# Optimization experiments

Hardware: AMD Instinct MI355X
Metric: run time of the kernel (lower is better)

## Reference

```python
import jax, jax.numpy as jnp
import numpy as np

NEG_SLOPE = 0.2  # PyG GATConv default LeakyReLU negative slope


def gat_conv(x, src, dst, W, att_src, att_dst, bias, heads, out_ch, concat):
    """PyG-style GATConv (eval mode, self-loops already appended to src/dst)."""
    n = x.shape[0]
    xh = (x @ W).reshape(n, heads, out_ch)          # [N, H, C]
    a_src = jnp.sum(xh * att_src, axis=-1)          # [N, H]
    a_dst = jnp.sum(xh * att_dst, axis=-1)          # [N, H]
    e = jax.nn.leaky_relu(a_src[src] + a_dst[dst], NEG_SLOPE)  # [E, H]
    # segment softmax over edges grouped by destination node
    m = jax.ops.segment_max(e, dst, num_segments=n)
    m = jnp.where(jnp.isfinite(m), m, 0.0)
    ex = jnp.exp(e - m[dst])
    denom = jax.ops.segment_sum(ex, dst, num_segments=n)
    alpha = ex / (denom[dst] + 1e-16)               # [E, H]
    msg = xh[src] * alpha[..., None]                # [E, H, C]
    out = jax.ops.segment_sum(msg, dst, num_segments=n)  # [N, H, C]
    out = out.reshape(n, heads * out_ch) if concat else out.mean(axis=1)
    return out + bias


def setup_inputs() -> dict:
    key = jax.random.key(0)
    ks = jax.random.split(key, 10)
    N, E, IN, OUT = 50000, 600000, 128, 64
    H1, C1 = 2, 2 * OUT   # conv1: heads=2, out=2*out_channels, concat -> 4*OUT
    H2, C2 = 1, OUT       # conv2: heads=1, concat=False
    s = 0.05
    return {
        "x": jax.random.normal(ks[0], (N, IN), dtype=jnp.float32),
        "edge_index": jax.random.randint(ks[1], (2, E), 0, N, dtype=jnp.int64),
        "W1": jax.random.normal(ks[2], (IN, H1 * C1), dtype=jnp.float32) * s,
        "att_src1": jax.random.normal(ks[3], (H1, C1), dtype=jnp.float32) * s,
        "att_dst1": jax.random.normal(ks[4], (H1, C1), dtype=jnp.float32) * s,
        "b1": jnp.zeros((H1 * C1,), dtype=jnp.float32),
        "W2": jax.random.normal(ks[5], (H1 * C1, H2 * C2), dtype=jnp.float32) * s,
        "att_src2": jax.random.normal(ks[6], (H2, C2), dtype=jnp.float32) * s,
        "att_dst2": jax.random.normal(ks[7], (H2, C2), dtype=jnp.float32) * s,
        "b2": jnp.zeros((C2,), dtype=jnp.float32),
    }


def reference(x, edge_index, W1, att_src1, att_dst1, b1, W2, att_src2, att_dst2, b2):
    n = x.shape[0]
    loop = jnp.arange(n, dtype=edge_index.dtype)
    src = jnp.concatenate([edge_index[0], loop])  # add_self_loops=True
    dst = jnp.concatenate([edge_index[1], loop])
    z = gat_conv(x, src, dst, W1, att_src1, att_dst1, b1, heads=2, out_ch=128, concat=True)
    z = jax.nn.relu(z)
    z = gat_conv(z, src, dst, W2, att_src2, att_dst2, b2, heads=1, out_ch=64, concat=False)
    # decode: dot product over original edge_index (no self loops)
    val = jnp.sum(z[edge_index[0]] * z[edge_index[1]], axis=-1)
    return val.reshape(-1)
```

## Files before the change

kernel.cpp:

```cpp
#include <hip/hip_runtime.h>
#include <math.h>

#define IN_F 128
#define F1 256
#define H1 2
#define F2 64
#define NEG 0.2f

typedef _Float16 f16x8 __attribute__((ext_vector_type(8)));
typedef _Float16 f16x4 __attribute__((ext_vector_type(4)));
typedef float f32x4 __attribute__((ext_vector_type(4)));

__global__ __launch_bounds__(256) void gemm1_mfma(
    const _Float16* __restrict__ Gh, const _Float16* __restrict__ Gl,
    const _Float16* __restrict__ Wth, const _Float16* __restrict__ Wtl,
    const float* __restrict__ b1,
    _Float16* __restrict__ zh, _Float16* __restrict__ zl, int N)
{
    __shared__ _Float16 BhF[32 * 64 * 8];
    __shared__ _Float16 BlF[32 * 64 * 8];
    int t = threadIdx.x;
    int h = blockIdx.y;
    const _Float16* wsh = Wth + (long)h * 128 * IN_F;
    const _Float16* wsl = Wtl + (long)h * 128 * IN_F;
    #pragma unroll
    for (int p = 0; p < 8; ++p) {
        int fs = p * 256 + t;
        int lane = fs & 63;
        int slot = fs >> 6;
        int ct = slot >> 2, ks = slot & 3;
        int col = ct * 16 + (lane & 15);
        int koff = ks * 32 + (lane >> 4) * 8;
        *(f16x8*)&BhF[fs * 8] = *(const f16x8*)&wsh[(long)col * IN_F + koff];
        *(f16x8*)&BlF[fs * 8] = *(const f16x8*)&wsl[(long)col * IN_F + koff];
    }
    __syncthreads();

    int wave = t >> 6, lane = t & 63;
    int quad = lane >> 4, l4 = lane & 15;
    int rt = blockIdx.x * 4 + wave;
    if (rt * 16 >= N) return;
    long mrow = (long)rt * 16 + l4;
    const _Float16* gh = Gh + mrow * F1 + h * 128 + quad * 8;
    const _Float16* gl = Gl + mrow * F1 + h * 128 + quad * 8;
    f16x8 ah[4], al[4];
    #pragma unroll
    for (int ks = 0; ks < 4; ++ks) {
        ah[ks] = *(const f16x8*)(gh + ks * 32);
        al[ks] = *(const f16x8*)(gl + ks * 32);
    }
    f32x4 acc[8];
    #pragma unroll
    for (int ct = 0; ct < 8; ++ct) acc[ct] = (f32x4){0.f, 0.f, 0.f, 0.f};
    #pragma unroll
    for (int ks = 0; ks < 4; ++ks) {
        #pragma unroll
        for (int ct = 0; ct < 8; ++ct) {
            f16x8 bh = *(const f16x8*)&BhF[((ct * 4 + ks) * 64 + lane) * 8];
            f16x8 bl = *(const f16x8*)&BlF[((ct * 4 + ks) * 64 + lane) * 8];
            acc[ct] = __builtin_amdgcn_mfma_f32_16x16x32_f16(ah[ks], bh, acc[ct], 0, 0, 0);
            acc[ct] = __builtin_amdgcn_mfma_f32_16x16x32_f16(al[ks], bh, acc[ct], 0, 0, 0);
            acc[ct] = __builtin_amdgcn_mfma_f32_16x16x32_f16(ah[ks], bl, acc[ct], 0, 0, 0);
        }
    }
    int rbase = rt * 16 + quad * 4;
    #pragma unroll
    for (int ct = 0; ct < 8; ++ct) {
        int col = h * 128 + ct * 16 + l4;
        float b1c = b1[col];
        #pragma unroll
        for (int i = 0; i < 4; ++i) {
            float v = fmaxf(acc[ct][i] + b1c, 0.f);
            _Float16 hi = (_Float16)v;
            long idx = (long)(rbase + i) * F1 + col;
            zh[idx] = hi;
            zl[idx] = (_Float16)(v - (float)hi);
        }
    }
}

__global__ __launch_bounds__(256) void gemm2_mfma(
    const _Float16* __restrict__ zh, const _Float16* __restrict__ zl,
    const _Float16* __restrict__ W2th, const _Float16* __restrict__ W2tl,
    const float* __restrict__ as2, const float* __restrict__ ad2,
    float* __restrict__ xh2, float* __restrict__ a_src, float* __restrict__ a_dst,
    int N)
{
    __shared__ _Float16 BhF[32 * 64 * 8];
    __shared__ _Float16 BlF[32 * 64 * 8];
    int t = threadIdx.x;
    #pragma unroll
    for (int p = 0; p < 8; ++p) {
        int fs = p * 256 + t;
        int lane = fs & 63;
        int slot = fs >> 6;
        int ct = slot >> 3, ks = slot & 7;
        int col = ct * 16 + (lane & 15);
        int koff = ks * 32 + (lane >> 4) * 8;
        *(f16x8*)&BhF[fs * 8] = *(const f16x8*)&W2th[(long)col * F1 + koff];
        *(f16x8*)&BlF[fs * 8] = *(const f16x8*)&W2tl[(long)col * F1 + koff];
    }
    __syncthreads();

    int wave = t >> 6, lane = t & 63;
    int quad = lane >> 4, l4 = lane & 15;
    int rt = blockIdx.x * 4 + wave;
    if (rt * 16 >= N) return;
    long mrow = (long)rt * 16 + l4;
    const _Float16* ap = zh + mrow * F1 + quad * 8;
    const _Float16* alp = zl + mrow * F1 + quad * 8;
    f16x8 ah[8], al[8];
    #pragma unroll
    for (int ks = 0; ks < 8; ++ks) {
        ah[ks] = *(const f16x8*)(ap + ks * 32);
        al[ks] = *(const f16x8*)(alp + ks * 32);
    }
    f32x4 acc[4];
    #pragma unroll
    for (int ct = 0; ct < 4; ++ct) acc[ct] = (f32x4){0.f, 0.f, 0.f, 0.f};
    #pragma unroll
    for (int ks = 0; ks < 8; ++ks) {
        #pragma unroll
        for (int ct = 0; ct < 4; ++ct) {
            f16x8 bh = *(const f16x8*)&BhF[((ct * 8 + ks) * 64 + lane) * 8];
            f16x8 bl = *(const f16x8*)&BlF[((ct * 8 + ks) * 64 + lane) * 8];
            acc[ct] = __builtin_amdgcn_mfma_f32_16x16x32_f16(ah[ks], bh, acc[ct], 0, 0, 0);
            acc[ct] = __builtin_amdgcn_mfma_f32_16x16x32_f16(al[ks], bh, acc[ct], 0, 0, 0);
            acc[ct] = __builtin_amdgcn_mfma_f32_16x16x32_f16(ah[ks], bl, acc[ct], 0, 0, 0);
        }
    }
    int rbase = rt * 16 + quad * 4;
    float ps[4] = {0, 0, 0, 0}, pd[4] = {0, 0, 0, 0};
    #pragma unroll
    for (int ct = 0; ct < 4; ++ct) {
        int col = ct * 16 + l4;
        float asv = as2[col], adv = ad2[col];
        #pragma unroll
        for (int i = 0; i < 4; ++i) {
            xh2[(long)(rbase + i) * F2 + col] = acc[ct][i];
            ps[i] = fmaf(acc[ct][i], asv, ps[i]);
            pd[i] = fmaf(acc[ct][i], adv, pd[i]);
        }
    }
    #pragma unroll
    for (int o = 1; o < 16; o <<= 1) {
        #pragma unroll
        for (int i = 0; i < 4; ++i) {
            ps[i] += __shfl_xor(ps[i], o);
            pd[i] += __shfl_xor(pd[i], o);
        }
    }
    if (l4 == 0) {
        #pragma unroll
        for (int i = 0; i < 4; ++i) {
            a_src[rbase + i] = ps[i];
            a_dst[rbase + i] = pd[i];
        }
    }
}

__global__ __launch_bounds__(256) void hist_uv_k(
    const int* __restrict__ ei_d, int* __restrict__ deg, int* __restrict__ pos,
    int E, int Ep, int NBH,
    const float* __restrict__ W1, const float* __restrict__ as1,
    const float* __restrict__ ad1, float* __restrict__ UV4,
    _Float16* __restrict__ Wth, _Float16* __restrict__ Wtl,
    const float* __restrict__ W2,
    _Float16* __restrict__ W2th, _Float16* __restrict__ W2tl)
{
    if ((int)blockIdx.x < NBH) {
        int i = blockIdx.x * 256 + threadIdx.x;
        if (i >= Ep) return;
        int d = (i < E) ? ei_d[i] : (i - E);
        pos[i] = atomicAdd(&deg[d], 1);
    } else if ((int)blockIdx.x == NBH) {
        int t = threadIdx.x;
        int k = t >> 1, h = t & 1;
        const float* wrow = W1 + (long)k * F1 + h * 128;
        const float* sa = as1 + h * 128;
        const float* da = ad1 + h * 128;
        float u = 0.f, v = 0.f;
        for (int c = 0; c < 128; ++c) {
            float w = wrow[c];
            u = fmaf(w, sa[c], u);
            v = fmaf(w, da[c], v);
        }
        UV4[k * 4 + h] = u;
        UV4[k * 4 + 2 + h] = v;
    } else if ((int)blockIdx.x == NBH + 1) {
        int n = threadIdx.x;
        for (int k = 0; k < IN_F; ++k) {
            float w = W1[(long)k * F1 + n];
            _Float16 hh = (_Float16)w;
            Wth[(long)n * IN_F + k] = hh;
            Wtl[(long)n * IN_F + k] = (_Float16)(w - (float)hh);
        }
    } else {
        int n = threadIdx.x;
        if (n < F2) {
            for (int k = 0; k < F1; ++k) {
                float w = W2[(long)k * F2 + n];
                _Float16 hh = (_Float16)w;
                W2th[(long)n * F1 + k] = hh;
                W2tl[(long)n * F1 + k] = (_Float16)(w - (float)hh);
            }
        }
    }
}

__global__ __launch_bounds__(1024) void scanA_att_k(
    const int* __restrict__ deg, int* __restrict__ rloc, int* __restrict__ bsum,
    int N, int NBLK,
    const float* __restrict__ x, const float* __restrict__ UV4,
    float* __restrict__ a_src, float* __restrict__ a_dst)
{
    if ((int)blockIdx.x < NBLK) {
        __shared__ int wsum[16];
        int t = threadIdx.x, lane = t & 63, w = t >> 6;
        int i = blockIdx.x * 1024 + t;
        int v = (i < N) ? deg[i] : 0;
        int incl = v;
        #pragma unroll
        for (int o = 1; o < 64; o <<= 1) {
            int nb = __shfl_up(incl, o);
            if (lane >= o) incl += nb;
        }
        if (lane == 63) wsum[w] = incl;
        __syncthreads();
        if (w == 0 && lane < 16) {
            int s = wsum[lane];
            #pragma unroll
            for (int o = 1; o < 16; o <<= 1) {
                int nb = __shfl_up(s, o);
                if (lane >= o) s += nb;
            }
            wsum[lane] = s;
        }
        __syncthreads();
        int woff = (w == 0) ? 0 : wsum[w - 1];
        if (i < N) rloc[i] = woff + incl - v;
        if (t == 1023) bsum[blockIdx.x] = woff + incl;
    } else {
        int wave = threadIdx.x >> 6, lane = threadIdx.x & 63;
        int n = ((int)blockIdx.x - NBLK) * 16 + wave;
        if (n >= N) return;
        float2 xv = ((const float2*)(x + (long)n * IN_F))[lane];
        float4 u0 = ((const float4*)UV4)[2 * lane];
        float4 u1 = ((const float4*)UV4)[2 * lane + 1];
        float p0 = xv.x * u0.x + xv.y * u1.x;
        float p1 = xv.x * u0.y + xv.y * u1.y;
        float p2 = xv.x * u0.z + xv.y * u1.z;
        float p3 = xv.x * u0.w + xv.y * u1.w;
        #pragma unroll
        for (int o = 32; o > 0; o >>= 1) {
            p0 += __shfl_xor(p0, o); p1 += __shfl_xor(p1, o);
            p2 += __shfl_xor(p2, o); p3 += __shfl_xor(p3, o);
        }
        if (lane == 0) {
            a_src[(long)n * 2 + 0] = p0; a_src[(long)n * 2 + 1] = p1;
            a_dst[(long)n * 2 + 0] = p2; a_dst[(long)n * 2 + 1] = p3;
        }
    }
}

__global__ __launch_bounds__(1024) void scat_fix_k(
    const int* __restrict__ ei_s, const int* __restrict__ ei_d,
    const int* __restrict__ rloc, const int* __restrict__ bsum,
    const int* __restrict__ pos, int* __restrict__ rowptr,
    int* __restrict__ csr_src, int* __restrict__ csr_eid,
    int E, int Ep, int N, int NBLK)
{
    __shared__ int bexs[64];
    __shared__ int tot_sh;
    int t = threadIdx.x;
    if (t < 64) {
        int v = (t < NBLK) ? bsum[t] : 0;
        int incl = v;
        #pragma unroll
        for (int o = 1; o < 64; o <<= 1) {
            int nb = __shfl_up(incl, o);
            if (t >= o) incl += nb;
        }
        bexs[t] = incl - v;
        if (t == NBLK - 1) tot_sh = incl;
    }
    __syncthreads();
    if ((int)blockIdx.x < NBLK) {
        int i = blockIdx.x * 1024 + t;
        if (i < N) rowptr[i] = rloc[i] + bexs[blockIdx.x];
        if ((int)blockIdx.x == NBLK - 1 && t == 0) rowptr[N] = tot_sh;
    } else {
        int i = ((int)blockIdx.x - NBLK) * 1024 + t;
        if (i >= Ep) return;
        int s = (i < E) ? ei_s[i] : (i - E);
        int d = (i < E) ? ei_d[i] : (i - E);
        int at = rloc[d] + bexs[d >> 10] + pos[i];
        csr_src[at] = s;
        csr_eid[at] = (i < E) ? i : -1;
    }
}

__global__ __launch_bounds__(256) void agg1x(
    const int* __restrict__ rowptr, const int* __restrict__ csr_src,
    const float* __restrict__ a_s, const float* __restrict__ a_d,
    const float* __restrict__ x, _Float16* __restrict__ Gh,
    _Float16* __restrict__ Gl, int N)
{
    int wave = threadIdx.x >> 6, lane = threadIdx.x & 63;
    int d = blockIdx.x * 4 + wave;
    if (d >= N) return;
    int row = rowptr[d], end = rowptr[d + 1];
    int h = lane >> 5, l5 = lane & 31;
    int g = lane >> 4, q = lane & 15;
    float adh = a_d[(long)d * 2 + h];
    float acc[2][2][4];
    #pragma unroll
    for (int s0 = 0; s0 < 2; ++s0)
        #pragma unroll
        for (int h0 = 0; h0 < 2; ++h0)
            #pragma unroll
            for (int p = 0; p < 4; ++p) acc[s0][h0][p] = 0.f;
    float den = 0.f;
    for (int base = row; base < end; base += 32) {
        int cnt = min(32, end - base);
        int sreg = 0; float e = 0.f;
        if (l5 < cnt) {
            sreg = csr_src[base + l5];
            float v = a_s[(long)sreg * 2 + h] + adh;
            v = (v > 0.f) ? v : NEG * v;
            e = expf(v);
            den += e;
        }
        int jmax = (cnt + 3) >> 2;
        for (int j = 0; j < jmax; j += 2) {
            int mA = 4 * j + g;
            int mB = mA + 4;
            int sA = __shfl(sreg, mA);
            int sB = __shfl(sreg, mB);
            float w0A = __shfl(e, mA);
            float w1A = __shfl(e, 32 | mA);
            float w0B = __shfl(e, mB);
            float w1B = __shfl(e, 32 | mB);
            const float* xpA = x + (long)sA * IN_F + q * 4;
            const float* xpB = x + (long)sB * IN_F + q * 4;
            float4 a0 = *(const float4*)(xpA);
            float4 a1 = *(const float4*)(xpA + 64);
            float4 b0 = *(const float4*)(xpB);
            float4 b1 = *(const float4*)(xpB + 64);
            acc[0][0][0] = fmaf(w0A, a0.x, acc[0][0][0]);
            acc[0][0][1] = fmaf(w0A, a0.y, acc[0][0][1]);
            acc[0][0][2] = fmaf(w0A, a0.z, acc[0][0][2]);
            acc[0][0][3] = fmaf(w0A, a0.w, acc[0][0][3]);
            acc[1][0][0] = fmaf(w0A, a1.x, acc[1][0][0]);
            acc[1][0][1] = fmaf(w0A, a1.y, acc[1][0][1]);
            acc[1][0][2] = fmaf(w0A, a1.z, acc[1][0][2]);
            acc[1][0][3] = fmaf(w0A, a1.w, acc[1][0][3]);
            acc[0][1][0] = fmaf(w1A, a0.x, acc[0][1][0]);
            acc[0][1][1] = fmaf(w1A, a0.y, acc[0][1][1]);
            acc[0][1][2] = fmaf(w1A, a0.z, acc[0][1][2]);
            acc[0][1][3] = fmaf(w1A, a0.w, acc[0][1][3]);
            acc[1][1][0] = fmaf(w1A, a1.x, acc[1][1][0]);
            acc[1][1][1] = fmaf(w1A, a1.y, acc[1][1][1]);
            acc[1][1][2] = fmaf(w1A, a1.z, acc[1][1][2]);
            acc[1][1][3] = fmaf(w1A, a1.w, acc[1][1][3]);
            acc[0][0][0] = fmaf(w0B, b0.x, acc[0][0][0]);
            acc[0][0][1] = fmaf(w0B, b0.y, acc[0][0][1]);
            acc[0][0][2] = fmaf(w0B, b0.z, acc[0][0][2]);
            acc[0][0][3] = fmaf(w0B, b0.w, acc[0][0][3]);
            acc[1][0][0] = fmaf(w0B, b1.x, acc[1][0][0]);
            acc[1][0][1] = fmaf(w0B, b1.y, acc[1][0][1]);
            acc[1][0][2] = fmaf(w0B, b1.z, acc[1][0][2]);
            acc[1][0][3] = fmaf(w0B, b1.w, acc[1][0][3]);
            acc[0][1][0] = fmaf(w1B, b0.x, acc[0][1][0]);
            acc[0][1][1] = fmaf(w1B, b0.y, acc[0][1][1]);
            acc[0][1][2] = fmaf(w1B, b0.z, acc[0][1][2]);
            acc[0][1][3] = fmaf(w1B, b0.w, acc[0][1][3]);
            acc[1][1][0] = fmaf(w1B, b1.x, acc[1][1][0]);
            acc[1][1][1] = fmaf(w1B, b1.y, acc[1][1][1]);
            acc[1][1][2] = fmaf(w1B, b1.z, acc[1][1][2]);
            acc[1][1][3] = fmaf(w1B, b1.w, acc[1][1][3]);
        }
    }
    #pragma unroll
    for (int o = 16; o > 0; o >>= 1) den += __shfl_xor(den, o);
    float den_o = __shfl_xor(den, 32);
    float den0 = (h == 0) ? den : den_o;
    float den1 = (h == 0) ? den_o : den;
    #pragma unroll
    for (int s0 = 0; s0 < 2; ++s0)
        #pragma unroll
        for (int h0 = 0; h0 < 2; ++h0)
            #pragma unroll
            for (int p = 0; p < 4; ++p) {
                float v = acc[s0][h0][p];
                v += __shfl_xor(v, 16);
                v += __shfl_xor(v, 32);
                acc[s0][h0][p] = v;
            }
    if (g == 0) {
        float inv0 = 1.0f / (den0 + 1e-16f);
        float inv1 = 1.0f / (den1 + 1e-16f);
        #pragma unroll
        for (int h0 = 0; h0 < 2; ++h0) {
            float inv = (h0 == 0) ? inv0 : inv1;
            #pragma unroll
            for (int s0 = 0; s0 < 2; ++s0) {
                f16x4 hi, lo;
                #pragma unroll
                for (int p = 0; p < 4; ++p) {
                    float v = acc[s0][h0][p] * inv;
                    hi[p] = (_Float16)v;
                    lo[p] = (_Float16)(v - (float)hi[p]);
                }
                long base = (long)d * F1 + h0 * 128 + s0 * 64 + q * 4;
                *(f16x4*)(Gh + base) = hi;
                *(f16x4*)(Gl + base) = lo;
            }
        }
    }
}

__global__ __launch_bounds__(256) void agg2_csr(
    const int* __restrict__ rowptr, const int* __restrict__ csr_src,
    const float* __restrict__ a_s, const float* __restrict__ a_d,
    const float* __restrict__ xh2, const float* __restrict__ b2,
    float* __restrict__ out2b, int N)
{
    int wave = threadIdx.x >> 6, lane = threadIdx.x & 63;
    int d = blockIdx.x * 4 + wave;
    if (d >= N) return;
    int row = rowptr[d], end = rowptr[d + 1];
    float adv = a_d[d];
    int g = lane >> 3, q = lane & 7;
    float acc[2][4] = {{0,0,0,0},{0,0,0,0}};
    float den = 0.f;
    for (int base = row; base < end; base += 64) {
        int cnt = min(64, end - base);
        float ev = 0.f; int sreg = 0;
        if (lane < cnt) {
            sreg = csr_src[base + lane];
            float v = a_s[sreg] + adv; v = (v > 0.f) ? v : NEG * v;
            ev = expf(v);
            den += ev;
        }
        int jmax = (cnt + 7) >> 3;
        for (int j = 0; j < jmax; j += 2) {
            int mA = 8 * j + g;
            int mB = mA + 8;
            int sA = __shfl(sreg, mA);
            int sB = __shfl(sreg, mB);
            float wA = __shfl(ev, mA);
            float wB = __shfl(ev, mB);
            const float* xpA = xh2 + (long)sA * F2 + q * 4;
            const float* xpB = xh2 + (long)sB * F2 + q * 4;
            float4 a0 = *(const float4*)(xpA);
            float4 a1 = *(const float4*)(xpA + 32);
            float4 b0 = *(const float4*)(xpB);
            float4 b1 = *(const float4*)(xpB + 32);
            acc[0][0] = fmaf(wA, a0.x, acc[0][0]); acc[0][1] = fmaf(wA, a0.y, acc[0][1]);
            acc[0][2] = fmaf(wA, a0.z, acc[0][2]); acc[0][3] = fmaf(wA, a0.w, acc[0][3]);
            acc[1][0] = fmaf(wA, a1.x, acc[1][0]); acc[1][1] = fmaf(wA, a1.y, acc[1][1]);
            acc[1][2] = fmaf(wA, a1.z, acc[1][2]); acc[1][3] = fmaf(wA, a1.w, acc[1][3]);
            acc[0][0] = fmaf(wB, b0.x, acc[0][0]); acc[0][1] = fmaf(wB, b0.y, acc[0][1]);
            acc[0][2] = fmaf(wB, b0.z, acc[0][2]); acc[0][3] = fmaf(wB, b0.w, acc[0][3]);
            acc[1][0] = fmaf(wB, b1.x, acc[1][0]); acc[1][1] = fmaf(wB, b1.y, acc[1][1]);
            acc[1][2] = fmaf(wB, b1.z, acc[1][2]); acc[1][3] = fmaf(wB, b1.w, acc[1][3]);
        }
    }
    #pragma unroll
    for (int o = 32; o > 0; o >>= 1) den += __shfl_xor(den, o);
    #pragma unroll
    for (int s0 = 0; s0 < 2; ++s0)
        #pragma unroll
        for (int p = 0; p < 4; ++p) {
            float v = acc[s0][p];
            v += __shfl_xor(v, 8);
            v += __shfl_xor(v, 16);
            v += __shfl_xor(v, 32);
            acc[s0][p] = v;
        }
    if (g == 0) {
        float inv = 1.0f / (den + 1e-16f);
        #pragma unroll
        for (int s0 = 0; s0 < 2; ++s0) {
            const float* bb = b2 + s0 * 32 + q * 4;
            float4 o4 = {acc[s0][0] * inv + bb[0], acc[s0][1] * inv + bb[1],
                         acc[s0][2] * inv + bb[2], acc[s0][3] * inv + bb[3]};
            *(float4*)(out2b + (long)d * F2 + s0 * 32 + q * 4) = o4;
        }
    }
}

__global__ __launch_bounds__(256) void decode_csr(
    const int* __restrict__ rowptr, const int* __restrict__ csr_src,
    const int* __restrict__ csr_eid, const float* __restrict__ z2b,
    float* __restrict__ out, int N)
{
    int wave = threadIdx.x >> 6, lane = threadIdx.x & 63;
    int d = blockIdx.x * 4 + wave;
    if (d >= N) return;
    int row = rowptr[d], end = rowptr[d + 1];
    int g = lane >> 3, q = lane & 7;
    const float* zd = z2b + (long)d * F2 + q * 4;
    float4 vd0 = *(const float4*)(zd);
    float4 vd1 = *(const float4*)(zd + 32);
    for (int base = row; base < end; base += 64) {
        int cnt = min(64, end - base);
        int sreg = 0, ereg = -1;
        if (lane < cnt) {
            sreg = csr_src[base + lane];
            ereg = csr_eid[base + lane];
        }
        int jmax = (cnt + 7) >> 3;
        for (int j = 0; j < jmax; j += 2) {
            int mA = 8 * j + g;
            int mB = mA + 8;
            int sA = __shfl(sreg, mA);
            int eA = __shfl(ereg, mA);
            int sB = __shfl(sreg, mB);
            int eB = __shfl(ereg, mB);
            const float* zsA = z2b + (long)sA * F2 + q * 4;
            const float* zsB = z2b + (long)sB * F2 + q * 4;
            float4 a0 = *(const float4*)(zsA);
            float4 a1 = *(const float4*)(zsA + 32);
            float4 b0 = *(const float4*)(zsB);
            float4 b1 = *(const float4*)(zsB + 32);
            float pA = vd0.x * a0.x + vd0.y * a0.y + vd0.z * a0.z + vd0.w * a0.w
                     + vd1.x * a1.x + vd1.y * a1.y + vd1.z * a1.z + vd1.w * a1.w;
            float pB = vd0.x * b0.x + vd0.y * b0.y + vd0.z * b0.z + vd0.w * b0.w
                     + vd1.x * b1.x + vd1.y * b1.y + vd1.z * b1.z + vd1.w * b1.w;
            pA += __shfl_xor(pA, 1);
            pB += __shfl_xor(pB, 1);
            pA += __shfl_xor(pA, 2);
            pB += __shfl_xor(pB, 2);
            pA += __shfl_xor(pA, 4);
            pB += __shfl_xor(pB, 4);
            if (q == 0 && eA >= 0) out[eA] = pA;
            if (q == 0 && eB >= 0) out[eB] = pB;
        }
    }
}

extern "C" void kernel_launch(void* const* d_in, const int* in_sizes, int n_in,
                              void* d_out, int out_size, void* d_ws, size_t ws_size,
                              hipStream_t stream) {
    const float* x   = (const float*)d_in[0];
    const int*   ei  = (const int*)d_in[1];
    const float* W1  = (const float*)d_in[2];
    const float* as1 = (const float*)d_in[3];
    const float* ad1 = (const float*)d_in[4];
    const float* b1  = (const float*)d_in[5];
    const float* W2  = (const float*)d_in[6];
    const float* as2 = (const float*)d_in[7];
    const float* ad2 = (const float*)d_in[8];
    const float* b2  = (const float*)d_in[9];

    int N  = in_sizes[0] / IN_F;
    int E  = in_sizes[1] / 2;
    int Ep = E + N;
    const int* ei_src = ei;
    const int* ei_dst = ei + E;

    float* ws = (float*)d_ws;
    size_t off = 0;
    auto alloc = [&](size_t n) { float* p = ws + off; off += (n + 63) & ~(size_t)63; return p; };

    _Float16* Gh   = (_Float16*)alloc((size_t)N * F1 / 2);
    _Float16* Gl   = (_Float16*)alloc((size_t)N * F1 / 2);
    _Float16* zh   = (_Float16*)alloc((size_t)N * F1 / 2);
    _Float16* zl   = (_Float16*)alloc((size_t)N * F1 / 2);
    _Float16* Wth  = (_Float16*)alloc(IN_F * F1 / 2);
    _Float16* Wtl  = (_Float16*)alloc(IN_F * F1 / 2);
    _Float16* W2th = (_Float16*)alloc(F1 * F2 / 2);
    _Float16* W2tl = (_Float16*)alloc(F1 * F2 / 2);
    float* xh2    = alloc((size_t)N * F2);
    float* out2b  = alloc((size_t)N * F2);
    float* a_src1 = alloc((size_t)N * H1);
    float* a_dst1 = alloc((size_t)N * H1);
    float* a_src2 = alloc(N);
    float* a_dst2 = alloc(N);
    float* UV4    = alloc(IN_F * 4);
    int* rowptr   = (int*)alloc(N + 64);
    int* rloc     = (int*)alloc(N + 64);
    int* csr_src  = (int*)alloc(Ep);
    int* csr_eid  = (int*)alloc(Ep);
    int* pos      = (int*)alloc(Ep);
    int* bsum     = (int*)alloc(64);
    int* deg      = (int*)alloc(N);
    hipMemsetAsync(deg, 0, (size_t)N * sizeof(int), stream);

    int NBLK = (N + 1023) / 1024;
    int NBH  = (Ep + 255) / 256;
    int NBS  = (Ep + 1023) / 1024;
    int NBA  = (N + 15) / 16;

    hist_uv_k<<<NBH + 3, 256, 0, stream>>>(ei_dst, deg, pos, E, Ep, NBH,
                                           W1, as1, ad1, UV4, Wth, Wtl,
                                           W2, W2th, W2tl);
    scanA_att_k<<<NBLK + NBA, 1024, 0, stream>>>(deg, rloc, bsum, N, NBLK,
                                                 x, UV4, a_src1, a_dst1);
    scat_fix_k<<<NBLK + NBS, 1024, 0, stream>>>(ei_src, ei_dst, rloc, bsum, pos,
                                                rowptr, csr_src, csr_eid,
                                                E, Ep, N, NBLK);

    agg1x<<<(N + 3) / 4, 256, 0, stream>>>(rowptr, csr_src, a_src1, a_dst1, x,
                                           Gh, Gl, N);
    gemm1_mfma<<<dim3((N + 63) / 64, 2), 256, 0, stream>>>(Gh, Gl, Wth, Wtl,
                                                           b1, zh, zl, N);

    gemm2_mfma<<<(N + 63) / 64, 256, 0, stream>>>(zh, zl, W2th, W2tl,
                                                  as2, ad2, xh2, a_src2, a_dst2, N);
    agg2_csr<<<(N + 3) / 4, 256, 0, stream>>>(rowptr, csr_src, a_src2, a_dst2, xh2, b2, out2b, N);

    decode_csr<<<(N + 3) / 4, 256, 0, stream>>>(rowptr, csr_src, csr_eid, out2b,
                                                (float*)d_out, N);
}
```

Before: 312.9 us.

## Precompute layer-1 attention weights and denominators during CSR scatter

Moves the layer-1 edge score computation (leaky-relu plus exp) and the softmax denominator into the CSR scatter kernel. It stores per-edge float2 weights in CSR order and accumulates denominators with atomics. The aggregation kernel then reads precomputed weights and no longer needs the shuffle-based weight broadcast or the denominator reduction. The cost is an extra per-edge float2 array in memory, global atomics per edge, an extra memset, and a different floating-point summation order for the denominators.

```diff
diff --git a/kernel.cpp b/kernel.cpp
--- a/kernel.cpp
+++ b/kernel.cpp
@@ -268,6 +268,8 @@
     const int* __restrict__ rloc, const int* __restrict__ bsum,
     const int* __restrict__ pos, int* __restrict__ rowptr,
     int* __restrict__ csr_src, int* __restrict__ csr_eid,
+    const float* __restrict__ as1v, const float* __restrict__ ad1v,
+    float2* __restrict__ csr_e, float* __restrict__ den1,
     int E, int Ep, int N, int NBLK)
 {
     __shared__ int bexs[64];
@@ -297,12 +299,20 @@
         int at = rloc[d] + bexs[d >> 10] + pos[i];
         csr_src[at] = s;
         csr_eid[at] = (i < E) ? i : -1;
+        float v0 = as1v[(long)s * 2 + 0] + ad1v[(long)d * 2 + 0];
+        float v1 = as1v[(long)s * 2 + 1] + ad1v[(long)d * 2 + 1];
+        v0 = (v0 > 0.f) ? v0 : NEG * v0;
+        v1 = (v1 > 0.f) ? v1 : NEG * v1;
+        float e0 = expf(v0), e1 = expf(v1);
+        csr_e[at] = make_float2(e0, e1);
+        atomicAdd(&den1[(long)d * 2 + 0], e0);
+        atomicAdd(&den1[(long)d * 2 + 1], e1);
     }
 }
 
 __global__ __launch_bounds__(256) void agg1x(
     const int* __restrict__ rowptr, const int* __restrict__ csr_src,
-    const float* __restrict__ a_s, const float* __restrict__ a_d,
+    const float2* __restrict__ csr_e, const float* __restrict__ den1,
     const float* __restrict__ x, _Float16* __restrict__ Gh,
     _Float16* __restrict__ Gl, int N)
 {
@@ -310,9 +320,7 @@
     int d = blockIdx.x * 4 + wave;
     if (d >= N) return;
     int row = rowptr[d], end = rowptr[d + 1];
-    int h = lane >> 5, l5 = lane & 31;
     int g = lane >> 4, q = lane & 15;
-    float adh = a_d[(long)d * 2 + h];
     float acc[2][2][4];
     #pragma unroll
     for (int s0 = 0; s0 < 2; ++s0)
@@ -320,72 +328,54 @@
         for (int h0 = 0; h0 < 2; ++h0)
             #pragma unroll
             for (int p = 0; p < 4; ++p) acc[s0][h0][p] = 0.f;
-    float den = 0.f;
-    for (int base = row; base < end; base += 32) {
-        int cnt = min(32, end - base);
-        int sreg = 0; float e = 0.f;
-        if (l5 < cnt) {
-            sreg = csr_src[base + l5];
-            float v = a_s[(long)sreg * 2 + h] + adh;
-            v = (v > 0.f) ? v : NEG * v;
-            e = expf(v);
-            den += e;
-        }
-        int jmax = (cnt + 3) >> 2;
-        for (int j = 0; j < jmax; j += 2) {
-            int mA = 4 * j + g;
-            int mB = mA + 4;
-            int sA = __shfl(sreg, mA);
-            int sB = __shfl(sreg, mB);
-            float w0A = __shfl(e, mA);
-            float w1A = __shfl(e, 32 | mA);
-            float w0B = __shfl(e, mB);
-            float w1B = __shfl(e, 32 | mB);
-            const float* xpA = x + (long)sA * IN_F + q * 4;
-            const float* xpB = x + (long)sB * IN_F + q * 4;
-            float4 a0 = *(const float4*)(xpA);
-            float4 a1 = *(const float4*)(xpA + 64);
-            float4 b0 = *(const float4*)(xpB);
-            float4 b1 = *(const float4*)(xpB + 64);
-            acc[0][0][0] = fmaf(w0A, a0.x, acc[0][0][0]);
-            acc[0][0][1] = fmaf(w0A, a0.y, acc[0][0][1]);
-            acc[0][0][2] = fmaf(w0A, a0.z, acc[0][0][2]);
-            acc[0][0][3] = fmaf(w0A, a0.w, acc[0][0][3]);
-            acc[1][0][0] = fmaf(w0A, a1.x, acc[1][0][0]);
-            acc[1][0][1] = fmaf(w0A, a1.y, acc[1][0][1]);
-            acc[1][0][2] = fmaf(w0A, a1.z, acc[1][0][2]);
-            acc[1][0][3] = fmaf(w0A, a1.w, acc[1][0][3]);
-            acc[0][1][0] = fmaf(w1A, a0.x, acc[0][1][0]);
-            acc[0][1][1] = fmaf(w1A, a0.y, acc[0][1][1]);
-            acc[0][1][2] = fmaf(w1A, a0.z, acc[0][1][2]);
-            acc[0][1][3] = fmaf(w1A, a0.w, acc[0][1][3]);
-            acc[1][1][0] = fmaf(w1A, a1.x, acc[1][1][0]);
-            acc[1][1][1] = fmaf(w1A, a1.y, acc[1][1][1]);
-            acc[1][1][2] = fmaf(w1A, a1.z, acc[1][1][2]);
-            acc[1][1][3] = fmaf(w1A, a1.w, acc[1][1][3]);
-            acc[0][0][0] = fmaf(w0B, b0.x, acc[0][0][0]);
-            acc[0][0][1] = fmaf(w0B, b0.y, acc[0][0][1]);
-            acc[0][0][2] = fmaf(w0B, b0.z, acc[0][0][2]);
-            acc[0][0][3] = fmaf(w0B, b0.w, acc[0][0][3]);
-            acc[1][0][0] = fmaf(w0B, b1.x, acc[1][0][0]);
-            acc[1][0][1] = fmaf(w0B, b1.y, acc[1][0][1]);
-            acc[1][0][2] = fmaf(w0B, b1.z, acc[1][0][2]);
-            acc[1][0][3] = fmaf(w0B, b1.w, acc[1][0][3]);
-            acc[0][1][0] = fmaf(w1B, b0.x, acc[0][1][0]);
-            acc[0][1][1] = fmaf(w1B, b0.y, acc[0][1][1]);
-            acc[0][1][2] = fmaf(w1B, b0.z, acc[0][1][2]);
-            acc[0][1][3] = fmaf(w1B, b0.w, acc[0][1][3]);
-            acc[1][1][0] = fmaf(w1B, b1.x, acc[1][1][0]);
-            acc[1][1][1] = fmaf(w1B, b1.y, acc[1][1][1]);
-            acc[1][1][2] = fmaf(w1B, b1.z, acc[1][1][2]);
-            acc[1][1][3] = fmaf(w1B, b1.w, acc[1][1][3]);
-        }
-    }
-    #pragma unroll
-    for (int o = 16; o > 0; o >>= 1) den += __shfl_xor(den, o);
-    float den_o = __shfl_xor(den, 32);
-    float den0 = (h == 0) ? den : den_o;
-    float den1 = (h == 0) ? den_o : den;
+    for (int m = row + g; m < end; m += 8) {
+        int sA = csr_src[m];
+        float2 eA = csr_e[m];
+        int mB = m + 4;
+        int sB = 0;
+        float2 eB = make_float2(0.f, 0.f);
+        if (mB < end) { sB = csr_src[mB]; eB = csr_e[mB]; }
+        const float* xpA = x + (long)sA * IN_F + q * 4;
+        const float* xpB = x + (long)sB * IN_F + q * 4;
+        float4 a0 = *(const float4*)(xpA);
+        float4 a1 = *(const float4*)(xpA + 64);
+        float4 b0 = *(const float4*)(xpB);
+        float4 b1 = *(const float4*)(xpB + 64);
+        float w0A = eA.x, w1A = eA.y;
+        float w0B = eB.x, w1B = eB.y;
+        acc[0][0][0] = fmaf(w0A, a0.x, acc[0][0][0]);
+        acc[0][0][1] = fmaf(w0A, a0.y, acc[0][0][1]);
+        acc[0][0][2] = fmaf(w0A, a0.z, acc[0][0][2]);
+        acc[0][0][3] = fmaf(w0A, a0.w, acc[0][0][3]);
+        acc[1][0][0] = fmaf(w0A, a1.x, acc[1][0][0]);
+        acc[1][0][1] = fmaf(w0A, a1.y, acc[1][0][1]);
+        acc[1][0][2] = fmaf(w0A, a1.z, acc[1][0][2]);
+        acc[1][0][3] = fmaf(w0A, a1.w, acc[1][0][3]);
+        acc[0][1][0] = fmaf(w1A, a0.x, acc[0][1][0]);
+        acc[0][1][1] = fmaf(w1A, a0.y, acc[0][1][1]);
+        acc[0][1][2] = fmaf(w1A, a0.z, acc[0][1][2]);
+        acc[0][1][3] = fmaf(w1A, a0.w, acc[0][1][3]);
+        acc[1][1][0] = fmaf(w1A, a1.x, acc[1][1][0]);
+        acc[1][1][1] = fmaf(w1A, a1.y, acc[1][1][1]);
+        acc[1][1][2] = fmaf(w1A, a1.z, acc[1][1][2]);
+        acc[1][1][3] = fmaf(w1A, a1.w, acc[1][1][3]);
+        acc[0][0][0] = fmaf(w0B, b0.x, acc[0][0][0]);
+        acc[0][0][1] = fmaf(w0B, b0.y, acc[0][0][1]);
+        acc[0][0][2] = fmaf(w0B, b0.z, acc[0][0][2]);
+        acc[0][0][3] = fmaf(w0B, b0.w, acc[0][0][3]);
+        acc[1][0][0] = fmaf(w0B, b1.x, acc[1][0][0]);
+        acc[1][0][1] = fmaf(w0B, b1.y, acc[1][0][1]);
+        acc[1][0][2] = fmaf(w0B, b1.z, acc[1][0][2]);
+        acc[1][0][3] = fmaf(w0B, b1.w, acc[1][0][3]);
+        acc[0][1][0] = fmaf(w1B, b0.x, acc[0][1][0]);
+        acc[0][1][1] = fmaf(w1B, b0.y, acc[0][1][1]);
+        acc[0][1][2] = fmaf(w1B, b0.z, acc[0][1][2]);
+        acc[0][1][3] = fmaf(w1B, b0.w, acc[0][1][3]);
+        acc[1][1][0] = fmaf(w1B, b1.x, acc[1][1][0]);
+        acc[1][1][1] = fmaf(w1B, b1.y, acc[1][1][1]);
+        acc[1][1][2] = fmaf(w1B, b1.z, acc[1][1][2]);
+        acc[1][1][3] = fmaf(w1B, b1.w, acc[1][1][3]);
+    }
     #pragma unroll
     for (int s0 = 0; s0 < 2; ++s0)
         #pragma unroll
@@ -398,8 +388,8 @@
                 acc[s0][h0][p] = v;
             }
     if (g == 0) {
-        float inv0 = 1.0f / (den0 + 1e-16f);
-        float inv1 = 1.0f / (den1 + 1e-16f);
+        float inv0 = 1.0f / (den1[(long)d * 2 + 0] + 1e-16f);
+        float inv1 = 1.0f / (den1[(long)d * 2 + 1] + 1e-16f);
         #pragma unroll
         for (int h0 = 0; h0 < 2; ++h0) {
             float inv = (h0 == 0) ? inv0 : inv1;
@@ -580,6 +570,8 @@
     float* a_src2 = alloc(N);
     float* a_dst2 = alloc(N);
     float* UV4    = alloc(IN_F * 4);
+    float2* csr_e = (float2*)alloc((size_t)Ep * 2);
+    float* den1   = alloc((size_t)N * 2);
     int* rowptr   = (int*)alloc(N + 64);
     int* rloc     = (int*)alloc(N + 64);
     int* csr_src  = (int*)alloc(Ep);
@@ -588,6 +580,7 @@
     int* bsum     = (int*)alloc(64);
     int* deg      = (int*)alloc(N);
     hipMemsetAsync(deg, 0, (size_t)N * sizeof(int), stream);
+    hipMemsetAsync(den1, 0, (size_t)N * 2 * sizeof(float), stream);
 
     int NBLK = (N + 1023) / 1024;
     int NBH  = (Ep + 255) / 256;
@@ -601,9 +594,10 @@
                                                  x, UV4, a_src1, a_dst1);
     scat_fix_k<<<NBLK + NBS, 1024, 0, stream>>>(ei_src, ei_dst, rloc, bsum, pos,
                                                 rowptr, csr_src, csr_eid,
+                                                a_src1, a_dst1, csr_e, den1,
                                                 E, Ep, N, NBLK);
 
-    agg1x<<<(N + 3) / 4, 256, 0, stream>>>(rowptr, csr_src, a_src1, a_dst1, x,
+    agg1x<<<(N + 3) / 4, 256, 0, stream>>>(rowptr, csr_src, csr_e, den1, x,
                                            Gh, Gl, N);
     gemm1_mfma<<<dim3((N + 63) / 64, 2), 256, 0, stream>>>(Gh, Gl, Wth, Wtl,
                                                            b1, zh, zl, N);
```

New measurement: 377.8 us. +20.7%, slower.
